# Kernel tuning notes

Hardware: AMD Instinct MI355X
Metric: run time of the kernel (lower is better)

## Reference

```python
import jax, jax.numpy as jnp
import numpy as np
from jax import lax

# Fixed-point scales (powers of two, as in linger's luna/venus pipeline).
# scale_gi = input_scale * weight_ih_scale, scale_gh = hidden_scale * weight_hh_scale.
SCALE_GI = 2.0 ** 14
SCALE_GH = 2.0 ** 14
Q27 = 2.0 ** 27
Q15 = 2.0 ** 15
Q31 = 2.0 ** 31
INT32_MIN = -(2.0 ** 31)
INT32_MAX = 2.0 ** 31 - 1


def quant_round(x, scale):
    # QuantMode.floor_add: floor(x*scale + 0.5)/scale, with straight-through gradient
    # (linger QAT rounding uses STE).
    q = jnp.floor(x * scale + 0.5) / scale
    return x + lax.stop_gradient(q - x)


@jax.custom_vjp
def qsigmoid(x):
    # Quantize input to Q27 int32, evaluate sigmoid, output Q31 -> requant to Q15.
    i_q27 = jnp.clip(jnp.floor(x * Q27 + 0.5), INT32_MIN, INT32_MAX)
    s = jax.nn.sigmoid(i_q27 / Q27)
    out_q31 = jnp.floor(s * Q31 + 0.5)
    out_q15 = jnp.floor(out_q31 * (2.0 ** -16) + 0.5)  # luna_requant(31 -> 15)
    return out_q15 / Q15

def _qsig_fwd(x):
    return qsigmoid(x), x

def _qsig_bwd(x, g):
    s = jax.nn.sigmoid(x)
    return (g * s * (1.0 - s),)

qsigmoid.defvjp(_qsig_fwd, _qsig_bwd)


@jax.custom_vjp
def qtanh(x):
    i_q27 = jnp.clip(jnp.floor(x * Q27 + 0.5), INT32_MIN, INT32_MAX)
    t = jnp.tanh(i_q27 / Q27)
    out_q31 = jnp.floor(t * Q31 + 0.5)
    out_q15 = jnp.floor(out_q31 * (2.0 ** -16) + 0.5)
    return out_q15 / Q15

def _qtanh_fwd(x):
    return qtanh(x), x

def _qtanh_bwd(x, g):
    t = jnp.tanh(x)
    return (g * (1.0 - t * t),)

qtanh.defvjp(_qtanh_fwd, _qtanh_bwd)


def setup_inputs() -> dict:
    key = jax.random.key(0)
    k = jax.random.split(key, 6)
    B, I, H = 8192, 512, 512
    return {
        "input_x": jax.random.normal(k[0], (B, I), dtype=jnp.float32),
        "hidden": jax.random.normal(k[1], (B, H), dtype=jnp.float32),
        "weight_ih": jax.random.normal(k[2], (3 * H, I), dtype=jnp.float32) * 0.05,
        "weight_hh": jax.random.normal(k[3], (3 * H, H), dtype=jnp.float32) * 0.05,
        "bias_ih": jax.random.normal(k[4], (3 * H,), dtype=jnp.float32) * 0.05,
        "bias_hh": jax.random.normal(k[5], (3 * H,), dtype=jnp.float32) * 0.05,
    }


def reference(input_x, hidden, weight_ih, weight_hh, bias_ih, bias_hh):
    # Dense gate projections: [B, 3H]
    gi = input_x @ weight_ih.T + bias_ih
    gh = hidden @ weight_hh.T + bias_hh
    # Requant gate pre-activations to fixed-point grid (biasih/biashh quantizers)
    gi = quant_round(gi, SCALE_GI)
    gh = quant_round(gh, SCALE_GH)
    i_r, i_i, i_n = jnp.split(gi, 3, axis=1)
    h_r, h_i, h_n = jnp.split(gh, 3, axis=1)
    resetgate = qsigmoid(i_r + h_r)
    inputgate = qsigmoid(i_i + h_i)
    # h_n requantized to Q27, reset*h_n product requantized to Q15
    h_n = quant_round(h_n, Q27)
    resetgate_h_n = quant_round(resetgate * h_n, Q15)
    newgate = qtanh(resetgate_h_n + i_n)
    new_hidden = quant_round(hidden, Q15)
    hy = newgate + inputgate * (new_hidden - newgate)
    return hy
```

## Files before the change

### kernel.cpp

```cpp
#include <hip/hip_runtime.h>
#include <math.h>


typedef _Float16 f16x8  __attribute__((ext_vector_type(8)));
typedef _Float16 f16x4  __attribute__((ext_vector_type(4)));
typedef __bf16   bf16x8 __attribute__((ext_vector_type(8)));
typedef float    f32x16 __attribute__((ext_vector_type(16)));

namespace {

constexpr int Bsz = 8192, Ksz = 512, Hsz = 512;
constexpr int BM = 64, BN = 64;

constexpr unsigned WCH0    = 16384u;
constexpr unsigned NCHUNK  = 16384u + 3072u;
constexpr unsigned WS_F16  = NCHUNK * 512u;
constexpr size_t   WS_NEED = (size_t)WS_F16 * 2;

constexpr int SLAB2 = 24576;

__device__ __forceinline__ float qround(float x, float s, float invs) {
    return floorf(x * s + 0.5f) * invs;
}

__device__ __forceinline__ float qsigmoid_dev(float x) {
    float iq = floorf(x * 134217728.0f + 0.5f);
    iq = fminf(fmaxf(iq, -2147483648.0f), 2147483648.0f);
    float e = __expf(-iq * 7.450580596923828125e-9f);
    float s = __builtin_amdgcn_rcpf(1.0f + e);
    float q31 = floorf(s * 2147483648.0f + 0.5f);
    float q15 = floorf(q31 * 1.52587890625e-5f + 0.5f);
    return q15 * 3.0517578125e-5f;
}

__device__ __forceinline__ float qtanh_dev(float x) {
    float iq = floorf(x * 134217728.0f + 0.5f);
    iq = fminf(fmaxf(iq, -2147483648.0f), 2147483648.0f);
    float z = iq * 7.450580596923828125e-9f;
    float e = __expf(2.0f * z);
    float t = 1.0f - 2.0f * __builtin_amdgcn_rcpf(e + 1.0f);
    float q31 = floorf(t * 2147483648.0f + 0.5f);
    float q15 = floorf(q31 * 1.52587890625e-5f + 0.5f);
    return q15 * 3.0517578125e-5f;
}

__device__ __forceinline__ void dma16(const void* g, void* l) {
    __builtin_amdgcn_global_load_lds(
        (const __attribute__((address_space(1))) unsigned int*)g,
        (__attribute__((address_space(3))) unsigned int*)l, 16, 0, 0);
}

__device__ __forceinline__ void split2(float a, float b, unsigned& hi, unsigned& lo) {
    unsigned ua = __float_as_uint(a); ua += 0x7fffu + ((ua >> 16) & 1u);
    unsigned ub = __float_as_uint(b); ub += 0x7fffu + ((ub >> 16) & 1u);
    hi = (ua >> 16) | (ub & 0xffff0000u);
    float ra = a - __uint_as_float(ua & 0xffff0000u);
    float rb = b - __uint_as_float(ub & 0xffff0000u);
    unsigned va = __float_as_uint(ra); va += 0x7fffu + ((va >> 16) & 1u);
    unsigned vb = __float_as_uint(rb); vb += 0x7fffu + ((vb >> 16) & 1u);
    lo = (va >> 16) | (vb & 0xffff0000u);
}

}

__global__ __launch_bounds__(256) void cvt_lds_f16(
    const float* __restrict__ x, const float* __restrict__ h,
    const float* __restrict__ wih, const float* __restrict__ whh,
    _Float16* __restrict__ ws)
{
    __shared__ __align__(16) _Float16 lt[8192];

    const int b2  = blockIdx.x;
    const int b   = b2 >> 1;
    const int kha = b2 & 1;
    const int tid = threadIdx.x;

    const float* src;
    unsigned chbase;
    if (b < 512) {
        const int arr = b >> 8, M32 = b & 255;
        src = (arr ? h : x) + (size_t)M32 * 32u * 512u;
        chbase = (unsigned)arr * 8192u + (unsigned)M32 * 32u;
    } else {
        const int w = b - 512;
        const int g = w >> 4, N32 = w & 15;
        const int rowLocal = (g % 3) * 512 + N32 * 32;
        src = (g < 3 ? wih : whh) + (size_t)rowLocal * 512u;
        chbase = WCH0 + (unsigned)((g * 16 + N32) * 32);
    }
    src += kha * 256;

#pragma unroll
    for (int rep = 0; rep < 8; ++rep) {
        const int idx = rep * 256 + tid;
        const int row = idx >> 6;
        const int q   = idx & 63;
        const float4 v = *(const float4*)(src + (size_t)row * 512 + q * 4);
        const int K16l = q >> 2;
        const int kh   = (q >> 1) & 1;
        const int half = (q & 1) * 4;
        const int rsw  = (row + (q >> 1)) & 31;
        f16x4 o;
        o[0] = (_Float16)v.x; o[1] = (_Float16)v.y;
        o[2] = (_Float16)v.z; o[3] = (_Float16)v.w;
        *(f16x4*)&lt[K16l * 512 + kh * 256 + rsw * 8 + half] = o;
    }
    __syncthreads();

    const int wid = tid >> 6, lane = tid & 63;
    const int kh  = lane >> 5, row = lane & 31;
#pragma unroll
    for (int cc = 0; cc < 4; ++cc) {
        const int K16l = wid * 4 + cc;
        const int rsw  = (row + 2 * K16l + kh) & 31;
        const f16x8 o = *(const f16x8*)&lt[K16l * 512 + kh * 256 + rsw * 8];
        *(f16x8*)(ws + (size_t)(chbase + (unsigned)(kha * 16 + K16l)) * 512u
                      + lane * 8) = o;
    }
}

__global__ __launch_bounds__(512, 2) void qgru_f16_dma6(
    const _Float16* __restrict__ ws, const float* __restrict__ hid,
    const float* __restrict__ bih, const float* __restrict__ bhh,
    float* __restrict__ out)
{
    __shared__ __align__(16) _Float16 lds[3 * SLAB2];

    const int t = threadIdx.x, lane = t & 63, wid = t >> 6;
    const int mt = wid >> 2, nt = wid & 3;

    const int bid = blockIdx.x;
    const int n0  = (bid & 3) * 128;
    const int m0  = (bid >> 2) * 128;

    unsigned goffW[6];
    int      ldstW[6];
#pragma unroll
    for (int c = 0; c < 6; ++c) {
        const int gi = wid * 6 + c;
        const int g = gi >> 3, n32 = (gi >> 1) & 3, ks2 = gi & 1;
        const unsigned ch = WCH0
            + (unsigned)((g * 16 + (n0 >> 5) + n32) * 32) + (unsigned)ks2;
        goffW[c] = ch * 1024u + (unsigned)lane * 16u;
        ldstW[c] = gi * 512;
    }

    unsigned offA[8];
#pragma unroll
    for (int i = 0; i < 8; ++i) {
        const int ks2 = i >> 2, arr = (i >> 1) & 1, mf = i & 1;
        const unsigned ch = (unsigned)arr * 8192u
            + (unsigned)((m0 >> 5) + mt * 2 + mf) * 32u + (unsigned)ks2;
        offA[i] = ch * 1024u + (unsigned)lane * 16u;
    }

    f32x16 acc[4][2];
#pragma unroll
    for (int cid = 0; cid < 4; ++cid)
#pragma unroll
        for (int mf = 0; mf < 2; ++mf)
#pragma unroll
            for (int i = 0; i < 16; ++i) acc[cid][mf][i] = 0.0f;

    const char* wsb = (const char*)ws;
    const int lr = lane & 31, lk8 = (lane >> 5) * 8;

    f16x8 aS[3][8];

#pragma unroll
    for (int b = 0; b < 2; ++b) {
        const unsigned kb = (unsigned)b * 2048u;
#pragma unroll
        for (int i = 0; i < 8; ++i)
            aS[b][i] = *(const f16x8*)(wsb + offA[i] + kb);
#pragma unroll
        for (int c = 0; c < 6; ++c)
            dma16(wsb + goffW[c] + kb, &lds[b * SLAB2 + ldstW[c]]);
    }

#pragma unroll
    for (int step = 0; step < 16; ++step) {
        const int cur = step % 3;

        if (step < 14) {
            const int nxt = (step + 2) % 3;
            const unsigned kb = (unsigned)(step + 2) * 2048u;
#pragma unroll
            for (int i = 0; i < 8; ++i)
                aS[nxt][i] = *(const f16x8*)(wsb + offA[i] + kb);
#pragma unroll
            for (int c = 0; c < 6; ++c)
                dma16(wsb + goffW[c] + kb, &lds[nxt * SLAB2 + ldstW[c]]);
            asm volatile("s_waitcnt vmcnt(28)" ::: "memory");
        } else if (step == 14) {
            asm volatile("s_waitcnt vmcnt(14)" ::: "memory");
        } else {
            asm volatile("s_waitcnt vmcnt(0)" ::: "memory");
        }
        __builtin_amdgcn_s_barrier();
        __builtin_amdgcn_s_setprio(1);

#pragma unroll
        for (int ks2 = 0; ks2 < 2; ++ks2) {
            const int base = cur * SLAB2 + lk8 * 32 + lr * 8;
#pragma unroll
            for (int g = 0; g < 6; ++g) {
                const f16x8 bv = *(const f16x8*)
                    &lds[base + (((g * 4 + nt) * 2 + ks2) * 512)];
                const int cid = (g < 3) ? g : (g == 5 ? 3 : g - 3);
                const int ab  = ks2 * 4 + ((g < 3) ? 0 : 2);
                acc[cid][0] = __builtin_amdgcn_mfma_f32_32x32x16_f16(
                                  aS[cur][ab + 0], bv, acc[cid][0], 0, 0, 0);
                acc[cid][1] = __builtin_amdgcn_mfma_f32_32x32x16_f16(
                                  aS[cur][ab + 1], bv, acc[cid][1], 0, 0, 0);
            }
        }

        __builtin_amdgcn_s_setprio(0);
        asm volatile("" ::: "memory");
        __builtin_amdgcn_s_barrier();
    }

    constexpr float S14 = 16384.0f,     I14 = 1.0f / 16384.0f;
    constexpr float S15 = 32768.0f,     I15 = 1.0f / 32768.0f;

    const int lh = lane >> 5, l32 = lane & 31;
    const int n = n0 + nt * 32 + l32;
    const float brc = bih[n] + bhh[n];
    const float bic = bih[n + 512] + bhh[n + 512];
    const float bnn = bih[n + 1024];
    const float cnn = bhh[n + 1024];

#pragma unroll
    for (int mf = 0; mf < 2; ++mf) {
#pragma unroll
        for (int r = 0; r < 16; ++r) {
            const int row = (r & 3) + 8 * (r >> 2) + 4 * lh;
            const int m   = m0 + mt * 64 + mf * 32 + row;
            const float hv = hid[(size_t)m * Hsz + n];
            const float rg  = qsigmoid_dev(qround(acc[0][mf][r] + brc, S14, I14));
            const float ig  = qsigmoid_dev(qround(acc[1][mf][r] + bic, S14, I14));
            const float gin = qround(acc[2][mf][r] + bnn, S14, I14);
            const float ghn = qround(acc[3][mf][r] + cnn, S14, I14);
            const float rh  = qround(rg * ghn, S15, I15);
            const float ng  = qtanh_dev(rh + gin);
            const float nh  = qround(hv, S15, I15);
            out[(size_t)m * Hsz + n] = ng + ig * (nh - ng);
        }
    }
}

__global__ __launch_bounds__(256, 2) void qgru_mfma_bf16x3(
    const float* __restrict__ x, const float* __restrict__ hid,
    const float* __restrict__ wih, const float* __restrict__ whh,
    const float* __restrict__ bih, const float* __restrict__ bhh,
    float* __restrict__ out)
{
    __shared__ __align__(16) unsigned short lds[16384];

    const int t = threadIdx.x, lane = t & 63, wid = t >> 6;
    const int mt = wid >> 1, nt = wid & 1;
    const int m0 = blockIdx.x * BM, n0 = blockIdx.y * BN;
    const int s_r = t >> 2, s_k = (t & 3) << 2;
    const int s_kh = s_k >> 3, s_j = s_k & 7, s_rt = s_r >> 5, s_r32 = s_r & 31;

    const float* gA[2];
    gA[0] = x   + (size_t)(m0 + s_r) * Ksz + s_k;
    gA[1] = hid + (size_t)(m0 + s_r) * Ksz + s_k;
    const float* gW[6];
#pragma unroll
    for (int g = 0; g < 3; ++g) {
        gW[g]     = wih + (size_t)(g * Hsz + n0 + s_r) * Ksz + s_k;
        gW[g + 3] = whh + (size_t)(g * Hsz + n0 + s_r) * Ksz + s_k;
    }
    const int lh = lane >> 5, l32 = lane & 31;

    f32x16 acc[6];
#pragma unroll
    for (int g = 0; g < 6; ++g)
#pragma unroll
        for (int i = 0; i < 16; ++i) acc[g][i] = 0.0f;

    float4 vA[2], vW[6];
#pragma unroll
    for (int tt = 0; tt < 2; ++tt) vA[tt] = *(const float4*)gA[tt];
#pragma unroll
    for (int g = 0; g < 6; ++g)    vW[g]  = *(const float4*)gW[g];

    for (int k0 = 0; k0 < Ksz; k0 += 16) {
        __syncthreads();
#pragma unroll
        for (int tt = 0; tt < 2; ++tt) {
            unsigned h0, h1, l0, l1;
            split2(vA[tt].x, vA[tt].y, h0, l0);
            split2(vA[tt].z, vA[tt].w, h1, l1);
            unsigned bH = ((((tt*2+0)*2+s_rt)*2+s_kh)*32+s_r32)*8 + s_j;
            unsigned bL = ((((tt*2+1)*2+s_rt)*2+s_kh)*32+s_r32)*8 + s_j;
            *reinterpret_cast<uint2*>(&lds[bH]) = make_uint2(h0, h1);
            *reinterpret_cast<uint2*>(&lds[bL]) = make_uint2(l0, l1);
        }
#pragma unroll
        for (int g = 0; g < 6; ++g) {
            unsigned h0, h1, l0, l1;
            split2(vW[g].x, vW[g].y, h0, l0);
            split2(vW[g].z, vW[g].w, h1, l1);
            unsigned bH = 4096u + ((((g*2+0)*2+s_rt)*2+s_kh)*32+s_r32)*8 + s_j;
            unsigned bL = 4096u + ((((g*2+1)*2+s_rt)*2+s_kh)*32+s_r32)*8 + s_j;
            *reinterpret_cast<uint2*>(&lds[bH]) = make_uint2(h0, h1);
            *reinterpret_cast<uint2*>(&lds[bL]) = make_uint2(l0, l1);
        }
        __syncthreads();
        const int kn = (k0 + 16 < Ksz) ? (k0 + 16) : 0;
#pragma unroll
        for (int tt = 0; tt < 2; ++tt) vA[tt] = *(const float4*)(gA[tt] + kn);
#pragma unroll
        for (int g = 0; g < 6; ++g)    vW[g]  = *(const float4*)(gW[g] + kn);

        const bf16x8 ax_hi = *reinterpret_cast<const bf16x8*>(&lds[((((0)*2+mt)*2+lh)*32+l32)*8]);
        const bf16x8 ax_lo = *reinterpret_cast<const bf16x8*>(&lds[((((1)*2+mt)*2+lh)*32+l32)*8]);
        const bf16x8 ah_hi = *reinterpret_cast<const bf16x8*>(&lds[((((2)*2+mt)*2+lh)*32+l32)*8]);
        const bf16x8 ah_lo = *reinterpret_cast<const bf16x8*>(&lds[((((3)*2+mt)*2+lh)*32+l32)*8]);
#pragma unroll
        for (int g = 0; g < 6; ++g) {
            const bf16x8 b_hi = *reinterpret_cast<const bf16x8*>(&lds[4096u + ((((g*2+0)*2+nt)*2+lh)*32+l32)*8]);
            const bf16x8 b_lo = *reinterpret_cast<const bf16x8*>(&lds[4096u + ((((g*2+1)*2+nt)*2+lh)*32+l32)*8]);
            const bf16x8 a_hi = (g < 3) ? ax_hi : ah_hi;
            const bf16x8 a_lo = (g < 3) ? ax_lo : ah_lo;
            acc[g] = __builtin_amdgcn_mfma_f32_32x32x16_bf16(a_hi, b_hi, acc[g], 0, 0, 0);
            acc[g] = __builtin_amdgcn_mfma_f32_32x32x16_bf16(a_hi, b_lo, acc[g], 0, 0, 0);
            acc[g] = __builtin_amdgcn_mfma_f32_32x32x16_bf16(a_lo, b_hi, acc[g], 0, 0, 0);
        }
    }

    constexpr float S14 = 16384.0f,     I14 = 1.0f / 16384.0f;
    constexpr float S15 = 32768.0f,     I15 = 1.0f / 32768.0f;
    constexpr float S27 = 134217728.0f, I27 = 1.0f / 134217728.0f;
    const int n = n0 + nt * 32 + l32;
    const float br = bih[n], bi = bih[n + 512], bn = bih[n + 1024];
    const float cr = bhh[n], ci = bhh[n + 512], cn = bhh[n + 1024];
#pragma unroll
    for (int r = 0; r < 16; ++r) {
        const int row = (r & 3) + 8 * (r >> 2) + 4 * lh;
        const int m   = m0 + mt * 32 + row;
        const float hv = hid[(size_t)m * Hsz + n];
        float gir = qround(acc[0][r] + br, S14, I14);
        float gii = qround(acc[1][r] + bi, S14, I14);
        float gin = qround(acc[2][r] + bn, S14, I14);
        float ghr = qround(acc[3][r] + cr, S14, I14);
        float ghi = qround(acc[4][r] + ci, S14, I14);
        float ghn = qround(acc[5][r] + cn, S14, I14);
        float resetg = qsigmoid_dev(gir + ghr);
        float inputg = qsigmoid_dev(gii + ghi);
        float hn  = qround(ghn, S27, I27);
        float rh  = qround(resetg * hn, S15, I15);
        float newg = qtanh_dev(rh + gin);
        float nh  = qround(hv, S15, I15);
        out[(size_t)m * Hsz + n] = newg + inputg * (nh - newg);
    }
}

extern "C" void kernel_launch(void* const* d_in, const int* in_sizes, int n_in,
                              void* d_out, int out_size, void* d_ws, size_t ws_size,
                              hipStream_t stream) {
    const float* x   = (const float*)d_in[0];
    const float* hid = (const float*)d_in[1];
    const float* wih = (const float*)d_in[2];
    const float* whh = (const float*)d_in[3];
    const float* bih = (const float*)d_in[4];
    const float* bhh = (const float*)d_in[5];
    float* out = (float*)d_out;

    if (ws_size >= WS_NEED) {
        cvt_lds_f16<<<1216, 256, 0, stream>>>(
            x, hid, wih, whh, (_Float16*)d_ws);
        qgru_f16_dma6<<<256, 512, 0, stream>>>(
            (const _Float16*)d_ws, hid, bih, bhh, out);
    } else {
        dim3 grid(Bsz / BM, Hsz / BN);
        qgru_mfma_bf16x3<<<grid, dim3(256), 0, stream>>>(
            x, hid, wih, whh, bih, bhh, out);
    }
}
```

Measured before the change: 134.4 us.

## Shrink GEMM tile to 128x64 with 512 blocks and fine-grained 8-phase pipeline

Changes the fused GRU GEMM kernel from 128x128 tiles on 256 blocks to 128x64 tiles on 512 blocks. Each wave now owns one 32x32 M fragment, and the K loop has 8 steps of 64, each split into 8 phases of three MFMAs. A-fragment register prefetch and weight DMA are interleaved with those phases, with barriers per phase. The aim is more parallelism (512 blocks on 256 CUs) and fewer accumulator registers per wave. The cost is more A-tile traffic per output, halved weight reuse, and many more barriers.

```diff
diff --git a/kernel.cpp b/kernel.cpp
--- a/kernel.cpp
+++ b/kernel.cpp
@@ -17,7 +17,7 @@
 constexpr unsigned WS_F16  = NCHUNK * 512u;
 constexpr size_t   WS_NEED = (size_t)WS_F16 * 2;
 
-constexpr int SLAB2 = 24576;
+constexpr int SLABF = 24576;
 
 __device__ __forceinline__ float qround(float x, float s, float invs) {
     return floorf(x * s + 0.5f) * invs;
@@ -119,106 +119,100 @@
     }
 }
 
-__global__ __launch_bounds__(512, 2) void qgru_f16_dma6(
+__global__ __launch_bounds__(512, 2) void qgru_f16_p8(
     const _Float16* __restrict__ ws, const float* __restrict__ hid,
     const float* __restrict__ bih, const float* __restrict__ bhh,
     float* __restrict__ out)
 {
-    __shared__ __align__(16) _Float16 lds[3 * SLAB2];
-
-    const int t = threadIdx.x, lane = t & 63, wid = t >> 6;
-    const int mt = wid >> 2, nt = wid & 3;
+    __shared__ __align__(16) _Float16 lds[3 * SLABF];
+
+    const int t512 = threadIdx.x, lane = t512 & 63, wid = t512 >> 6;
+    const int mt = wid >> 1, nt = wid & 1;
 
     const int bid = blockIdx.x;
-    const int n0  = (bid & 3) * 128;
-    const int m0  = (bid >> 2) * 128;
+    const int n0  = (bid & 7) * 64;
+    const int m0  = (bid >> 3) * 128;
 
     unsigned goffW[6];
     int      ldstW[6];
 #pragma unroll
     for (int c = 0; c < 6; ++c) {
         const int gi = wid * 6 + c;
-        const int g = gi >> 3, n32 = (gi >> 1) & 3, ks2 = gi & 1;
+        const int g = gi >> 3, n32 = (gi >> 2) & 1, k16 = gi & 3;
         const unsigned ch = WCH0
-            + (unsigned)((g * 16 + (n0 >> 5) + n32) * 32) + (unsigned)ks2;
+            + (unsigned)((g * 16 + (n0 >> 5) + n32) * 32) + (unsigned)k16;
         goffW[c] = ch * 1024u + (unsigned)lane * 16u;
         ldstW[c] = gi * 512;
     }
 
-    unsigned offA[8];
-#pragma unroll
-    for (int i = 0; i < 8; ++i) {
-        const int ks2 = i >> 2, arr = (i >> 1) & 1, mf = i & 1;
+    unsigned offAb[2];
+#pragma unroll
+    for (int arr = 0; arr < 2; ++arr) {
         const unsigned ch = (unsigned)arr * 8192u
-            + (unsigned)((m0 >> 5) + mt * 2 + mf) * 32u + (unsigned)ks2;
-        offA[i] = ch * 1024u + (unsigned)lane * 16u;
-    }
-
-    f32x16 acc[4][2];
+            + (unsigned)(((m0 >> 5) + mt) * 32);
+        offAb[arr] = ch * 1024u + (unsigned)lane * 16u;
+    }
+
+    f32x16 acc[4];
 #pragma unroll
     for (int cid = 0; cid < 4; ++cid)
 #pragma unroll
-        for (int mf = 0; mf < 2; ++mf)
-#pragma unroll
-            for (int i = 0; i < 16; ++i) acc[cid][mf][i] = 0.0f;
+        for (int i = 0; i < 16; ++i) acc[cid][i] = 0.0f;
 
     const char* wsb = (const char*)ws;
-    const int lr = lane & 31, lk8 = (lane >> 5) * 8;
-
-    f16x8 aS[3][8];
-
-#pragma unroll
-    for (int b = 0; b < 2; ++b) {
-        const unsigned kb = (unsigned)b * 2048u;
-#pragma unroll
-        for (int i = 0; i < 8; ++i)
-            aS[b][i] = *(const f16x8*)(wsb + offA[i] + kb);
+
+    f16x8 aS[2][8];
+
+#pragma unroll
+    for (int i = 0; i < 8; ++i)
+        aS[0][i] = *(const f16x8*)(wsb + offAb[i & 1] + (unsigned)((i >> 1) * 1024));
+#pragma unroll
+    for (int b = 0; b < 2; ++b)
 #pragma unroll
         for (int c = 0; c < 6; ++c)
-            dma16(wsb + goffW[c] + kb, &lds[b * SLAB2 + ldstW[c]]);
-    }
-
-#pragma unroll
-    for (int step = 0; step < 16; ++step) {
-        const int cur = step % 3;
-
-        if (step < 14) {
-            const int nxt = (step + 2) % 3;
-            const unsigned kb = (unsigned)(step + 2) * 2048u;
-#pragma unroll
-            for (int i = 0; i < 8; ++i)
-                aS[nxt][i] = *(const f16x8*)(wsb + offA[i] + kb);
-#pragma unroll
-            for (int c = 0; c < 6; ++c)
-                dma16(wsb + goffW[c] + kb, &lds[nxt * SLAB2 + ldstW[c]]);
-            asm volatile("s_waitcnt vmcnt(28)" ::: "memory");
-        } else if (step == 14) {
-            asm volatile("s_waitcnt vmcnt(14)" ::: "memory");
-        } else {
-            asm volatile("s_waitcnt vmcnt(0)" ::: "memory");
+            dma16(wsb + goffW[c] + (unsigned)(b * 4096),
+                  &lds[b * SLABF + ldstW[c]]);
+    asm volatile("s_waitcnt vmcnt(6)" ::: "memory");
+    __builtin_amdgcn_s_barrier();
+
+#pragma unroll
+    for (int t = 0; t < 8; ++t) {
+        const int cur  = t % 3;
+        const int nxtw = (t + 2) % 3;
+#pragma unroll
+        for (int ph = 0; ph < 8; ++ph) {
+            const int k16 = ph >> 1, h = ph & 1;
+            const int rbase = cur * SLABF + k16 * 512 + lane * 8;
+            const f16x8 b0 = *(const f16x8*)&lds[rbase + (((3*h+0)*2 + nt) * 2048)];
+            const f16x8 b1 = *(const f16x8*)&lds[rbase + (((3*h+1)*2 + nt) * 2048)];
+            const f16x8 b2 = *(const f16x8*)&lds[rbase + (((3*h+2)*2 + nt) * 2048)];
+            if (t < 7)
+                aS[(t + 1) & 1][ph] = *(const f16x8*)
+                    (wsb + offAb[h] + (unsigned)((t + 1) * 4096 + k16 * 1024));
+            if (ph == 7) {
+                if (t < 6) {
+#pragma unroll
+                    for (int c = 0; c < 6; ++c)
+                        dma16(wsb + goffW[c] + (unsigned)((t + 2) * 4096),
+                              &lds[nxtw * SLABF + ldstW[c]]);
+                    asm volatile("s_waitcnt vmcnt(6)" ::: "memory");
+                } else if (t == 6) {
+                    asm volatile("s_waitcnt vmcnt(0)" ::: "memory");
+                }
+            }
+            __builtin_amdgcn_s_barrier();
+            asm volatile("s_waitcnt lgkmcnt(0)" ::: "memory");
+            __builtin_amdgcn_s_setprio(1);
+            const int cid2 = h ? 3 : 2;
+            acc[0]    = __builtin_amdgcn_mfma_f32_32x32x16_f16(
+                            aS[t & 1][ph], b0, acc[0], 0, 0, 0);
+            acc[1]    = __builtin_amdgcn_mfma_f32_32x32x16_f16(
+                            aS[t & 1][ph], b1, acc[1], 0, 0, 0);
+            acc[cid2] = __builtin_amdgcn_mfma_f32_32x32x16_f16(
+                            aS[t & 1][ph], b2, acc[cid2], 0, 0, 0);
+            __builtin_amdgcn_s_setprio(0);
+            __builtin_amdgcn_s_barrier();
         }
-        __builtin_amdgcn_s_barrier();
-        __builtin_amdgcn_s_setprio(1);
-
-#pragma unroll
-        for (int ks2 = 0; ks2 < 2; ++ks2) {
-            const int base = cur * SLAB2 + lk8 * 32 + lr * 8;
-#pragma unroll
-            for (int g = 0; g < 6; ++g) {
-                const f16x8 bv = *(const f16x8*)
-                    &lds[base + (((g * 4 + nt) * 2 + ks2) * 512)];
-                const int cid = (g < 3) ? g : (g == 5 ? 3 : g - 3);
-                const int ab  = ks2 * 4 + ((g < 3) ? 0 : 2);
-                acc[cid][0] = __builtin_amdgcn_mfma_f32_32x32x16_f16(
-                                  aS[cur][ab + 0], bv, acc[cid][0], 0, 0, 0);
-                acc[cid][1] = __builtin_amdgcn_mfma_f32_32x32x16_f16(
-                                  aS[cur][ab + 1], bv, acc[cid][1], 0, 0, 0);
-            }
-        }
-
-        __builtin_amdgcn_s_setprio(0);
-        asm volatile("" ::: "memory");
-        __builtin_amdgcn_s_barrier();
     }
 
     constexpr float S14 = 16384.0f,     I14 = 1.0f / 16384.0f;
@@ -232,21 +226,18 @@
     const float cnn = bhh[n + 1024];
 
 #pragma unroll
-    for (int mf = 0; mf < 2; ++mf) {
-#pragma unroll
-        for (int r = 0; r < 16; ++r) {
-            const int row = (r & 3) + 8 * (r >> 2) + 4 * lh;
-            const int m   = m0 + mt * 64 + mf * 32 + row;
-            const float hv = hid[(size_t)m * Hsz + n];
-            const float rg  = qsigmoid_dev(qround(acc[0][mf][r] + brc, S14, I14));
-            const float ig  = qsigmoid_dev(qround(acc[1][mf][r] + bic, S14, I14));
-            const float gin = qround(acc[2][mf][r] + bnn, S14, I14);
-            const float ghn = qround(acc[3][mf][r] + cnn, S14, I14);
-            const float rh  = qround(rg * ghn, S15, I15);
-            const float ng  = qtanh_dev(rh + gin);
-            const float nh  = qround(hv, S15, I15);
-            out[(size_t)m * Hsz + n] = ng + ig * (nh - ng);
-        }
+    for (int r = 0; r < 16; ++r) {
+        const int row = (r & 3) + 8 * (r >> 2) + 4 * lh;
+        const int m   = m0 + mt * 32 + row;
+        const float hv = hid[(size_t)m * Hsz + n];
+        const float rg  = qsigmoid_dev(qround(acc[0][r] + brc, S14, I14));
+        const float ig  = qsigmoid_dev(qround(acc[1][r] + bic, S14, I14));
+        const float gin = qround(acc[2][r] + bnn, S14, I14);
+        const float ghn = qround(acc[3][r] + cnn, S14, I14);
+        const float rh  = qround(rg * ghn, S15, I15);
+        const float ng  = qtanh_dev(rh + gin);
+        const float nh  = qround(hv, S15, I15);
+        out[(size_t)m * Hsz + n] = ng + ig * (nh - ng);
     }
 }
 
@@ -373,7 +364,7 @@
     if (ws_size >= WS_NEED) {
         cvt_lds_f16<<<1216, 256, 0, stream>>>(
             x, hid, wih, whh, (_Float16*)d_ws);
-        qgru_f16_dma6<<<256, 512, 0, stream>>>(
+        qgru_f16_p8<<<512, 512, 0, stream>>>(
             (const _Float16*)d_ws, hid, bih, bhh, out);
     } else {
         dim3 grid(Bsz / BM, Hsz / BN);
```

Result: no change. 134.1 us (-0.3%).
